# Optimization experiments

Hardware: AMD Instinct MI355X
Metric: run time of the kernel (lower is better)

Reference implementation:

```python
import jax, jax.numpy as jnp
import numpy as np

EPSILON = 0.1
ALPHA = 0.5
N_ITER = 10
N_USERS = 100000


def setup_inputs() -> dict:
    key = jax.random.key(0)
    k1, k2, k3, k4, k5, k6 = jax.random.split(key, 6)
    B, C, F = 2048, 1024, 128
    users = jax.random.randint(k1, (B,), 0, N_USERS)
    items = jax.random.randint(k2, (B, C), 0, C)
    D = jax.random.uniform(k3, (B, C), minval=0.1, maxval=1.0)
    capacities = jax.random.uniform(k4, (C,), minval=0.5, maxval=1.5)
    # ScaledEmbedding: normal init scaled down by embedding_dim
    item_emb = jax.random.normal(k5, (C, F), dtype=jnp.float32) / F
    user_emb = jax.random.normal(k6, (N_USERS, F), dtype=jnp.float32) / F
    return dict(users=users, items=items, D=D, capacities=capacities,
                item_emb=item_emb, user_emb=user_emb)


def reference(users, items, D, capacities, item_emb, user_emb):
    B, C = D.shape
    ie = item_emb[items]            # [B, C, F] gathered candidate embeddings
    ue = user_emb[users]            # [B, F]
    dot = jnp.einsum('bcf,bf->bc', ie, ue)          # batched dot products
    affinity = (1.0 - ALPHA) * dot - ALPHA * (D / jnp.mean(D))
    K = jnp.exp(affinity / EPSILON)                 # [B, C]

    scaling = B / N_USERS
    a = jnp.ones((B,), K.dtype)
    b = capacities * scaling                        # [C]

    def step(carry, _):
        _, v = carry
        u = a / (K @ v)                             # [B]
        v_new = b / (K.T @ u)                       # [C]
        return (u, v_new), None

    (u, v), _ = jax.lax.scan(step, (a, jnp.ones((C,), K.dtype)),
                             None, length=N_ITER)
    P = K * (u[:, None] * v[None, :])               # K * outer(u, v)
    return P
```

## Files before the change

kernel.cpp:

```cpp
#include <hip/hip_runtime.h>
#include <hip/hip_fp16.h>

#define BB      2048
#define CC      1024
#define FF      128
#define NBLK    256
#define RPB     8
#define TPB     512
#define NITER   10
#define SUBR    8
#define SCALING_F (2048.0f / 100000.0f)

__device__ __align__(16) __half g_Kh[BB * CC];
__device__ float g_meanPart[NBLK];
__device__ float g_colsum[NITER * SUBR * CC];

__global__ void __launch_bounds__(TPB)
k0_prep(const float* __restrict__ D) {
    const int bid = blockIdx.x, tid = threadIdx.x;
    for (int i = bid * TPB + tid; i < NITER * SUBR * CC; i += NBLK * TPB)
        g_colsum[i] = 0.0f;
    const float4* D4 = (const float4*)D;
    float p = 0.0f;
    for (int i = bid * TPB + tid; i < BB * CC / 4; i += NBLK * TPB) {
        float4 d = D4[i];
        p += d.x + d.y + d.z + d.w;
    }
    #pragma unroll
    for (int off = 32; off > 0; off >>= 1) p += __shfl_down(p, off, 64);
    __shared__ float red[TPB / 64];
    if ((tid & 63) == 0) red[tid >> 6] = p;
    __syncthreads();
    if (tid == 0) {
        float s = 0.0f;
        #pragma unroll
        for (int k = 0; k < TPB / 64; ++k) s += red[k];
        g_meanPart[bid] = s;
    }
}

__global__ void __launch_bounds__(TPB)
k1_buildK(const int* __restrict__ users, const int* __restrict__ items,
          const float* __restrict__ D, const float* __restrict__ iemb,
          const float* __restrict__ uemb) {
    const int bid = blockIdx.x, tid = threadIdx.x;
    const int r0 = bid * RPB;

    __shared__ float  uesh[RPB][FF];
    __shared__ __half dott[RPB][CC];
    __shared__ float  s2sh;

    if (tid < 256) {
        int r = tid >> 5, f4 = tid & 31;
        int u = users[r0 + r];
        ((float4*)uesh[r])[f4] = ((const float4*)(uemb + (size_t)u * FF))[f4];
    }
    if (tid < 64) {
        float s = g_meanPart[tid] + g_meanPart[tid + 64] +
                  g_meanPart[tid + 128] + g_meanPart[tid + 192];
        #pragma unroll
        for (int off = 32; off > 0; off >>= 1) s += __shfl_down(s, off, 64);
        if (tid == 0) s2sh = 5.0f * (float)(BB * CC) / s;
    }
    __syncthreads();

    const float4* us = (const float4*)uesh;
    #pragma unroll
    for (int jj = 0; jj < CC / TPB; ++jj) {
        int j = jj * TPB + tid;
        float acc[RPB] = {};
        const float4* ip = (const float4*)(iemb + (size_t)j * FF);
        for (int f4 = 0; f4 < FF / 4; ++f4) {
            float4 a = ip[f4];
            #pragma unroll
            for (int r = 0; r < RPB; ++r) {
                float4 b = us[r * (FF / 4) + f4];
                acc[r] += a.x * b.x + a.y * b.y + a.z * b.z + a.w * b.w;
            }
        }
        #pragma unroll
        for (int r = 0; r < RPB; ++r) dott[r][j] = __float2half(acc[r]);
    }
    __syncthreads();

    const float s2 = s2sh;
    const int4*   it4 = (const int4*)(items + ((size_t)r0 << 10));
    const float4* D4  = (const float4*)(D + ((size_t)r0 << 10));
    uint2* K2 = (uint2*)(g_Kh + ((size_t)r0 << 10));
    for (int i = tid; i < RPB * CC / 4; i += TPB) {
        int4 iv = it4[i];
        float4 d = D4[i];
        int r = i >> 8;
        float4 kv;
        kv.x = __expf(5.0f * __half2float(dott[r][iv.x]) - s2 * d.x);
        kv.y = __expf(5.0f * __half2float(dott[r][iv.y]) - s2 * d.y);
        kv.z = __expf(5.0f * __half2float(dott[r][iv.z]) - s2 * d.z);
        kv.w = __expf(5.0f * __half2float(dott[r][iv.w]) - s2 * d.w);
        __half2 lo = __floats2half2_rn(kv.x, kv.y);
        __half2 hi = __floats2half2_rn(kv.z, kv.w);
        uint2 o;
        o.x = *reinterpret_cast<unsigned*>(&lo);
        o.y = *reinterpret_cast<unsigned*>(&hi);
        K2[i] = o;
    }
}

__global__ void __launch_bounds__(TPB)
k_iter(const float* __restrict__ caps, int t) {
    const int bid = blockIdx.x, tid = threadIdx.x;
    const int r0 = bid * RPB;

    __shared__ float vsh[CC];
    __shared__ float ush[RPB];

    for (int c = tid; c < CC; c += TPB) {
        float v = 1.0f;
        if (t > 0) {
            const float* base = g_colsum + (size_t)(t - 1) * SUBR * CC;
            float s = 0.0f;
            #pragma unroll
            for (int k = 0; k < SUBR; ++k) s += base[k * CC + c];
            v = caps[c] * SCALING_F / s;
        }
        vsh[c] = v;
    }
    __syncthreads();

    {
        int w = tid >> 6, l = tid & 63;
        const __half2* kr = (const __half2*)(g_Kh + ((size_t)(r0 + w) << 10));
        const float2*  v2 = (const float2*)vsh;
        float p = 0.0f;
        #pragma unroll
        for (int i = 0; i < 8; ++i) {
            float2 k = __half22float2(kr[l + 64 * i]);
            float2 v = v2[l + 64 * i];
            p += k.x * v.x + k.y * v.y;
        }
        #pragma unroll
        for (int off = 32; off > 0; off >>= 1) p += __shfl_xor(p, off, 64);
        if (l == 0) ush[w] = 1.0f / p;
    }
    __syncthreads();

    {
        float sx = 0.0f, sy = 0.0f;
        #pragma unroll
        for (int r = 0; r < RPB; ++r) {
            const __half2* kp =
                (const __half2*)(g_Kh + ((size_t)(r0 + r) << 10)) + tid;
            float2 k = __half22float2(*kp);
            float ur = ush[r];
            sx += k.x * ur; sy += k.y * ur;
        }
        float* cb = g_colsum + ((size_t)t * SUBR + (bid & (SUBR - 1))) * CC
                  + 2 * tid;
        atomicAdd(cb, sx);
        atomicAdd(cb + 1, sy);
    }
}

__global__ void __launch_bounds__(TPB)
k_final(const float* __restrict__ caps, float* __restrict__ out) {
    const int bid = blockIdx.x, tid = threadIdx.x;
    const int r0 = bid * RPB;

    __shared__ float vsh[CC];
    __shared__ float ush[RPB];

    for (int c = tid; c < CC; c += TPB) {
        const float* base = g_colsum + (size_t)(NITER - 2) * SUBR * CC;
        float s = 0.0f;
        #pragma unroll
        for (int k = 0; k < SUBR; ++k) s += base[k * CC + c];
        vsh[c] = caps[c] * SCALING_F / s;
    }
    __syncthreads();

    {
        int w = tid >> 6, l = tid & 63;
        const __half2* kr = (const __half2*)(g_Kh + ((size_t)(r0 + w) << 10));
        const float2*  v2 = (const float2*)vsh;
        float p = 0.0f;
        #pragma unroll
        for (int i = 0; i < 8; ++i) {
            float2 k = __half22float2(kr[l + 64 * i]);
            float2 v = v2[l + 64 * i];
            p += k.x * v.x + k.y * v.y;
        }
        #pragma unroll
        for (int off = 32; off > 0; off >>= 1) p += __shfl_xor(p, off, 64);
        if (l == 0) ush[w] = 1.0f / p;
    }
    __syncthreads();

    for (int c = tid; c < CC; c += TPB) {
        const float* base = g_colsum + (size_t)(NITER - 1) * SUBR * CC;
        float s = 0.0f;
        #pragma unroll
        for (int k = 0; k < SUBR; ++k) s += base[k * CC + c];
        vsh[c] = caps[c] * SCALING_F / s;
    }
    __syncthreads();

    {
        float2 v = *(const float2*)&vsh[2 * tid];
        #pragma unroll
        for (int r = 0; r < RPB; ++r) {
            const __half2* kp =
                (const __half2*)(g_Kh + ((size_t)(r0 + r) << 10)) + tid;
            float2 k = __half22float2(*kp);
            float ur = ush[r];
            float2 p; p.x = k.x * ur * v.x; p.y = k.y * ur * v.y;
            ((float2*)(out + ((size_t)(r0 + r) << 10)))[tid] = p;
        }
    }
}

extern "C" void kernel_launch(void* const* d_in, const int* in_sizes, int n_in,
                              void* d_out, int out_size, void* d_ws, size_t ws_size,
                              hipStream_t stream) {
    const int*   users = (const int*)d_in[0];
    const int*   items = (const int*)d_in[1];
    const float* D     = (const float*)d_in[2];
    const float* caps  = (const float*)d_in[3];
    const float* iemb  = (const float*)d_in[4];
    const float* uemb  = (const float*)d_in[5];
    float* out = (float*)d_out;

    hipLaunchKernelGGL(k0_prep,   dim3(NBLK), dim3(TPB), 0, stream, D);
    hipLaunchKernelGGL(k1_buildK, dim3(NBLK), dim3(TPB), 0, stream,
                       users, items, D, iemb, uemb);
    for (int t = 0; t < NITER; ++t)
        hipLaunchKernelGGL(k_iter, dim3(NBLK), dim3(TPB), 0, stream, caps, t);
    hipLaunchKernelGGL(k_final,  dim3(NBLK), dim3(TPB), 0, stream, caps, out);
}
```

Measured before the change: 204.6 us.

## Store K in fp32 and stage rows in registers/LDS for reuse

Switches the K matrix from half to float storage and loads each block's K rows once into registers, before the v reduction. Those rows are then staged into shared memory for the column pass. k_final keeps K in registers and writes float4 outputs. This removes the duplicate global read of K per iteration and the half conversions, but doubles the bytes of K stored and read, and adds 32KB of shared memory per block.

```diff
diff --git a/kernel.cpp b/kernel.cpp
--- a/kernel.cpp
+++ b/kernel.cpp
@@ -11,7 +11,7 @@
 #define SUBR    8
 #define SCALING_F (2048.0f / 100000.0f)
 
-__device__ __align__(16) __half g_Kh[BB * CC];
+__device__ __align__(16) float g_K[BB * CC];
 __device__ float g_meanPart[NBLK];
 __device__ float g_colsum[NITER * SUBR * CC];
 
@@ -86,7 +86,7 @@
     const float s2 = s2sh;
     const int4*   it4 = (const int4*)(items + ((size_t)r0 << 10));
     const float4* D4  = (const float4*)(D + ((size_t)r0 << 10));
-    uint2* K2 = (uint2*)(g_Kh + ((size_t)r0 << 10));
+    float4*       K4  = (float4*)(g_K + ((size_t)r0 << 10));
     for (int i = tid; i < RPB * CC / 4; i += TPB) {
         int4 iv = it4[i];
         float4 d = D4[i];
@@ -96,12 +96,7 @@
         kv.y = __expf(5.0f * __half2float(dott[r][iv.y]) - s2 * d.y);
         kv.z = __expf(5.0f * __half2float(dott[r][iv.z]) - s2 * d.z);
         kv.w = __expf(5.0f * __half2float(dott[r][iv.w]) - s2 * d.w);
-        __half2 lo = __floats2half2_rn(kv.x, kv.y);
-        __half2 hi = __floats2half2_rn(kv.z, kv.w);
-        uint2 o;
-        o.x = *reinterpret_cast<unsigned*>(&lo);
-        o.y = *reinterpret_cast<unsigned*>(&hi);
-        K2[i] = o;
+        K4[i] = kv;
     }
 }
 
@@ -109,9 +104,16 @@
 k_iter(const float* __restrict__ caps, int t) {
     const int bid = blockIdx.x, tid = threadIdx.x;
     const int r0 = bid * RPB;
-
+    const int w = tid >> 6, l = tid & 63;
+
+    __shared__ float Kt[RPB][CC];
     __shared__ float vsh[CC];
     __shared__ float ush[RPB];
+
+    const float4* kr = (const float4*)(g_K + ((size_t)(r0 + w) << 10));
+    float4 k4[4];
+    #pragma unroll
+    for (int j = 0; j < 4; ++j) k4[j] = kr[l + 64 * j];
 
     for (int c = tid; c < CC; c += TPB) {
         float v = 1.0f;
@@ -127,15 +129,14 @@
     __syncthreads();
 
     {
-        int w = tid >> 6, l = tid & 63;
-        const __half2* kr = (const __half2*)(g_Kh + ((size_t)(r0 + w) << 10));
-        const float2*  v2 = (const float2*)vsh;
+        const float4* v4 = (const float4*)vsh;
+        float4* KtF4 = (float4*)Kt[w];
         float p = 0.0f;
         #pragma unroll
-        for (int i = 0; i < 8; ++i) {
-            float2 k = __half22float2(kr[l + 64 * i]);
-            float2 v = v2[l + 64 * i];
-            p += k.x * v.x + k.y * v.y;
+        for (int j = 0; j < 4; ++j) {
+            float4 v = v4[l + 64 * j];
+            p += k4[j].x * v.x + k4[j].y * v.y + k4[j].z * v.z + k4[j].w * v.w;
+            KtF4[l + 64 * j] = k4[j];
         }
         #pragma unroll
         for (int off = 32; off > 0; off >>= 1) p += __shfl_xor(p, off, 64);
@@ -147,9 +148,7 @@
         float sx = 0.0f, sy = 0.0f;
         #pragma unroll
         for (int r = 0; r < RPB; ++r) {
-            const __half2* kp =
-                (const __half2*)(g_Kh + ((size_t)(r0 + r) << 10)) + tid;
-            float2 k = __half22float2(*kp);
+            float2 k = *(const float2*)&Kt[r][2 * tid];
             float ur = ush[r];
             sx += k.x * ur; sy += k.y * ur;
         }
@@ -164,9 +163,14 @@
 k_final(const float* __restrict__ caps, float* __restrict__ out) {
     const int bid = blockIdx.x, tid = threadIdx.x;
     const int r0 = bid * RPB;
+    const int w = tid >> 6, l = tid & 63;
 
     __shared__ float vsh[CC];
-    __shared__ float ush[RPB];
+
+    const float4* kr = (const float4*)(g_K + ((size_t)(r0 + w) << 10));
+    float4 k4[4];
+    #pragma unroll
+    for (int j = 0; j < 4; ++j) k4[j] = kr[l + 64 * j];
 
     for (int c = tid; c < CC; c += TPB) {
         const float* base = g_colsum + (size_t)(NITER - 2) * SUBR * CC;
@@ -177,20 +181,18 @@
     }
     __syncthreads();
 
-    {
-        int w = tid >> 6, l = tid & 63;
-        const __half2* kr = (const __half2*)(g_Kh + ((size_t)(r0 + w) << 10));
-        const float2*  v2 = (const float2*)vsh;
+    float u;
+    {
+        const float4* v4 = (const float4*)vsh;
         float p = 0.0f;
         #pragma unroll
-        for (int i = 0; i < 8; ++i) {
-            float2 k = __half22float2(kr[l + 64 * i]);
-            float2 v = v2[l + 64 * i];
-            p += k.x * v.x + k.y * v.y;
+        for (int j = 0; j < 4; ++j) {
+            float4 v = v4[l + 64 * j];
+            p += k4[j].x * v.x + k4[j].y * v.y + k4[j].z * v.z + k4[j].w * v.w;
         }
         #pragma unroll
         for (int off = 32; off > 0; off >>= 1) p += __shfl_xor(p, off, 64);
-        if (l == 0) ush[w] = 1.0f / p;
+        u = 1.0f / p;
     }
     __syncthreads();
 
@@ -204,15 +206,15 @@
     __syncthreads();
 
     {
-        float2 v = *(const float2*)&vsh[2 * tid];
-        #pragma unroll
-        for (int r = 0; r < RPB; ++r) {
-            const __half2* kp =
-                (const __half2*)(g_Kh + ((size_t)(r0 + r) << 10)) + tid;
-            float2 k = __half22float2(*kp);
-            float ur = ush[r];
-            float2 p; p.x = k.x * ur * v.x; p.y = k.y * ur * v.y;
-            ((float2*)(out + ((size_t)(r0 + r) << 10)))[tid] = p;
+        const float4* v4 = (const float4*)vsh;
+        float4* o4 = (float4*)(out + ((size_t)(r0 + w) << 10));
+        #pragma unroll
+        for (int j = 0; j < 4; ++j) {
+            float4 v = v4[l + 64 * j];
+            float4 p;
+            p.x = k4[j].x * u * v.x;  p.y = k4[j].y * u * v.y;
+            p.z = k4[j].z * u * v.z;  p.w = k4[j].w * u * v.w;
+            o4[l + 64 * j] = p;
         }
     }
 }
```

Measured after the change: 193.1 us. 5.7% less time.
